# Performance work log

Measured on AMD Instinct MI355X. Metric: run time of the kernel, lower is better.

## Reference

```python
import jax, jax.numpy as jnp
import numpy as np

H, DK, DV, BS = 8, 64, 64, 128


def setup_inputs() -> dict:
    key = jax.random.key(0)
    ks = jax.random.split(key, 6)
    B, T, D = 2, 8193, 1024
    inner = H * DK
    x = jax.random.normal(ks[0], (B, T, D), jnp.float32)
    s = 0.02
    Wq = jax.random.normal(ks[1], (D, inner), jnp.float32) * s
    Wk = jax.random.normal(ks[2], (D, inner), jnp.float32) * s
    Wv = jax.random.normal(ks[3], (D, H * DV), jnp.float32) * s
    Wo = jax.random.normal(ks[4], (H * DV, D), jnp.float32) * s
    bo = jnp.zeros((D,), jnp.float32)
    return {"x": x, "Wq": Wq, "Wk": Wk, "Wv": Wv, "Wo": Wo, "bo": bo}


def _bigbird(x, Wq, Wk, Wv, Wo, bo):
    B, T, D = x.shape
    N = T - 1
    nb = N // BS
    scale = 1.0 / jnp.sqrt(jnp.asarray(DK, x.dtype))
    # projections -> (B, H, T, d)
    q = (x @ Wq).reshape(B, T, H, DK).transpose(0, 2, 1, 3)
    k = (x @ Wk).reshape(B, T, H, DK).transpose(0, 2, 1, 3)
    v = (x @ Wv).reshape(B, T, H, DV).transpose(0, 2, 1, 3)

    # global token (position 0) attends to everything
    sg = jnp.einsum('bhd,bhtd->bht', q[:, :, 0], k) * scale
    pg = jax.nn.softmax(sg, axis=-1)
    out_g = jnp.einsum('bht,bhtd->bhd', pg, v)  # (B,H,DV)

    kg = k[:, :, 0]  # (B,H,DK)
    vg = v[:, :, 0]  # (B,H,DV)
    qx = q[:, :, 1:].reshape(B, H, nb, BS, DK)
    kx = k[:, :, 1:].reshape(B, H, nb, BS, DK)
    vx = v[:, :, 1:].reshape(B, H, nb, BS, DV)

    # zero-pad one block on each side (faithful to original: zero blocks, not masked)
    kp = jnp.pad(kx, ((0, 0), (0, 0), (1, 1), (0, 0), (0, 0)))
    vp = jnp.pad(vx, ((0, 0), (0, 0), (1, 1), (0, 0), (0, 0)))
    k_local = jnp.concatenate([kp[:, :, 0:nb], kp[:, :, 1:nb + 1], kp[:, :, 2:nb + 2]], axis=3)
    v_local = jnp.concatenate([vp[:, :, 0:nb], vp[:, :, 1:nb + 1], vp[:, :, 2:nb + 2]], axis=3)

    kg_e = jnp.broadcast_to(kg[:, :, None, None, :], (B, H, nb, 1, DK))
    vg_e = jnp.broadcast_to(vg[:, :, None, None, :], (B, H, nb, 1, DV))
    k_full = jnp.concatenate([kg_e, k_local], axis=3)  # (B,H,nb,1+3BS,DK)
    v_full = jnp.concatenate([vg_e, v_local], axis=3)

    scores = jnp.einsum('bhnqd,bhnkd->bhnqk', qx, k_full) * scale
    p = jax.nn.softmax(scores, axis=-1)
    out_x = jnp.einsum('bhnqk,bhnkd->bhnqd', p, v_full).reshape(B, H, N, DV)

    out = jnp.concatenate([out_g[:, :, None, :], out_x], axis=2)  # (B,H,T,DV)
    out = out.transpose(0, 2, 1, 3).reshape(B, T, H * DV)
    return out @ Wo + bo


def reference(x, Wq, Wk, Wv, Wo, bo):
    return _bigbird(x, Wq, Wk, Wv, Wo, bo)
```

## Files before the change

### kernel.cpp

```cpp
#include <hip/hip_runtime.h>
#include <hip/hip_bf16.h>

#define T_TOK 8193
#define MROWS 16386
#define NBLK  64
#define GCH   16
#define GCS   513

typedef __attribute__((ext_vector_type(8))) short bf16x8;
typedef __attribute__((ext_vector_type(4))) float f32x4;
typedef unsigned short u16;
typedef unsigned int   u32;

__device__ __forceinline__ float blo(u32 u){ return __uint_as_float(u << 16); }
__device__ __forceinline__ float bhi(u32 u){ return __uint_as_float(u & 0xffff0000u); }
__device__ __forceinline__ u16 f2b(float f){
  u32 u = __float_as_uint(f);
  u = (u + 0x7fffu + ((u >> 16) & 1u)) >> 16;
  return (u16)u;
}
__device__ __forceinline__ float b2f(u16 v){ return __uint_as_float(((u32)v) << 16); }

#define GLDS16(gsrc, ldst) \
  __builtin_amdgcn_global_load_lds((const __attribute__((address_space(1))) void*)(gsrc), \
                                   (__attribute__((address_space(3))) void*)(ldst), 16, 0, 0)

__global__ __launch_bounds__(256)
void convx(const float* __restrict__ x, u16* __restrict__ xb)
{
  const size_t i = (size_t)blockIdx.x * 256 + threadIdx.x;
  const float4* p = (const float4*)x + i * 2;
  float4 a = p[0], b = p[1];
  uint4 st;
  st.x = (u32)f2b(a.x) | ((u32)f2b(a.y) << 16);
  st.y = (u32)f2b(a.z) | ((u32)f2b(a.w) << 16);
  st.z = (u32)f2b(b.x) | ((u32)f2b(b.y) << 16);
  st.w = (u32)f2b(b.z) | ((u32)f2b(b.w) << 16);
  *(uint4*)(xb + i * 8) = st;
}

__global__ __launch_bounds__(256)
void transposeW(const float* __restrict__ B0, const float* __restrict__ B1,
                const float* __restrict__ B2, int bpart,
                u16* __restrict__ outT, int K)
{
  __shared__ float tile[64][65];
  const int n0 = blockIdx.x * 64;
  const int k0 = blockIdx.y * 64;
  const int tx = threadIdx.x & 63;
  const int ty = threadIdx.x >> 6;
  const int part = n0 / bpart;
  const float* Bm = part == 0 ? B0 : (part == 1 ? B1 : B2);
  const int bn = n0 - part * bpart;
  #pragma unroll
  for (int i = 0; i < 16; ++i) {
    int k = i * 4 + ty;
    tile[tx][k] = Bm[(size_t)(k0 + k) * bpart + bn + tx];
  }
  __syncthreads();
  #pragma unroll
  for (int i = 0; i < 16; ++i) {
    int r = i * 4 + ty;
    outT[(size_t)(n0 + r) * K + k0 + tx] = f2b(tile[r][tx]);
  }
}

template<bool OUT_F32>
__global__ __launch_bounds__(512, 4)
void gemmk(const u16* __restrict__ A, const u16* __restrict__ BT,
           void* __restrict__ Cp, const float* __restrict__ bias,
           int M, int K, int ntm, int ntn, int ldc)
{
  __shared__ u16 lds[36864];
  const int tid  = threadIdx.x;
  const int lane = tid & 63;
  const int wid  = tid >> 6;
  const int l15  = lane & 15;
  const int g    = lane >> 4;
  const int wm   = (wid >> 1) * 64;
  const int wn   = (wid & 1) * 64;

  const int nwg  = gridDim.x;
  const int orig = blockIdx.x;
  const int q8 = nwg >> 3, r8 = nwg & 7;
  const int xcd = orig & 7, loc = orig >> 3;
  const int wg = (xcd < r8 ? xcd * (q8 + 1) : r8 * (q8 + 1) + (xcd - r8) * q8) + loc;
  const int GT  = 4;
  const int gsz = GT * ntn;
  const int tg  = wg / gsz;
  const int rem = wg - tg * gsz;
  const int gt  = (ntm - tg * GT < GT) ? (ntm - tg * GT) : GT;
  const int tn  = rem / gt;
  const int tml = rem - tn * gt;
  const int bm0 = (tg * GT + tml) * 256;
  const int bn0 = tn * 128;

  f32x4 acc[4][4];
  #pragma unroll
  for (int i = 0; i < 4; ++i)
    #pragma unroll
    for (int j = 0; j < 4; ++j) { f32x4 z = {0.f,0.f,0.f,0.f}; acc[i][j] = z; }

  const int rr   = tid >> 2;
  const int ch   = tid & 3;
  const int srcq = (ch ^ ((rr >> 1) & 3)) * 8;
  int ar0 = bm0 + rr;        if (ar0 >= M) ar0 = M - 1;
  int ar1 = bm0 + 128 + rr;  if (ar1 >= M) ar1 = M - 1;
  const u32 aOff0 = (u32)ar0 * (u32)K + srcq;
  const u32 aOff1 = (u32)ar1 * (u32)K + srcq;
  const u32 bOff  = (u32)(bn0 + rr) * (u32)K + srcq;
  const int ld8   = tid * 8;

#define STG(BUF, KO) do { \
    GLDS16(A + aOff0 + (KO), &lds[(BUF) * 12288 + ld8]); \
    GLDS16(A + aOff1 + (KO), &lds[(BUF) * 12288 + 4096 + ld8]); \
    GLDS16(BT + bOff + (KO), &lds[(BUF) * 12288 + 8192 + ld8]); \
  } while (0)

  const int ca = (g ^ ((l15 >> 1) & 3)) * 8;

  STG(0, 0);
  STG(1, 32);
  asm volatile("s_waitcnt vmcnt(3)" ::: "memory");
  __builtin_amdgcn_s_barrier();

  const int nt = K >> 5;
  int bufc = 0, bufn = 2;
  for (int t = 0; t < nt; ++t) {
    const int base = bufc * 12288;
    const bool more = (t + 2 < nt);
    bf16x8 bfr[4], af[2];
    #pragma unroll
    for (int ni = 0; ni < 4; ++ni)
      bfr[ni] = *(const bf16x8*)&lds[base + 8192 + (wn + ni * 16 + l15) * 32 + ca];
    af[0] = *(const bf16x8*)&lds[base + (wm + l15) * 32 + ca];
    af[1] = *(const bf16x8*)&lds[base + (wm + 16 + l15) * 32 + ca];
    if (more) STG(bufn, (t + 2) * 32);
    __builtin_amdgcn_s_barrier();
    __builtin_amdgcn_s_setprio(1);
    #pragma unroll
    for (int mi = 0; mi < 2; ++mi)
      #pragma unroll
      for (int ni = 0; ni < 4; ++ni)
        acc[mi][ni] = __builtin_amdgcn_mfma_f32_16x16x32_bf16(af[mi], bfr[ni], acc[mi][ni], 0, 0, 0);
    __builtin_amdgcn_s_setprio(0);
    __builtin_amdgcn_s_barrier();
    af[0] = *(const bf16x8*)&lds[base + (wm + 32 + l15) * 32 + ca];
    af[1] = *(const bf16x8*)&lds[base + (wm + 48 + l15) * 32 + ca];
    __builtin_amdgcn_s_barrier();
    __builtin_amdgcn_s_setprio(1);
    #pragma unroll
    for (int mi = 0; mi < 2; ++mi)
      #pragma unroll
      for (int ni = 0; ni < 4; ++ni)
        acc[2 + mi][ni] = __builtin_amdgcn_mfma_f32_16x16x32_bf16(af[mi], bfr[ni], acc[2 + mi][ni], 0, 0, 0);
    __builtin_amdgcn_s_setprio(0);
    if (more) asm volatile("s_waitcnt vmcnt(3)" ::: "memory");
    else      asm volatile("s_waitcnt vmcnt(0)" ::: "memory");
    __builtin_amdgcn_s_barrier();
    bufc = (bufc + 1 == 3) ? 0 : bufc + 1;
    bufn = (bufn + 1 == 3) ? 0 : bufn + 1;
  }
#undef STG

  #pragma unroll
  for (int mi = 0; mi < 4; ++mi) {
    #pragma unroll
    for (int r = 0; r < 4; ++r) {
      int grow = bm0 + wm + mi * 16 + g * 4 + r;
      if (grow >= M) continue;
      #pragma unroll
      for (int ni = 0; ni < 4; ++ni) {
        int gcol  = bn0 + wn + ni * 16 + l15;
        float val = acc[mi][ni][r];
        if (OUT_F32) ((float*)Cp)[(size_t)grow * ldc + gcol] = val + bias[gcol];
        else         ((u16*)Cp)[(size_t)grow * ldc + gcol]   = f2b(val);
      }
    }
  }
}

__global__ __launch_bounds__(256)
void gsplit(const u16* __restrict__ qkv, float* __restrict__ gbuf)
{
  const int c   = blockIdx.x & 15;
  const int h   = (blockIdx.x >> 4) & 7;
  const int b   = blockIdx.x >> 7;
  const int tid = threadIdx.x;
  const int lane = tid & 63;
  const int wid  = tid >> 6;
  const int t0 = c * GCS;
  const int t1 = (t0 + GCS < T_TOK) ? (t0 + GCS) : T_TOK;
  const int nt = t1 - t0;

  __shared__ float sc[GCS];
  __shared__ float q0s[64];
  __shared__ float wredm[4], wreds[4];
  __shared__ float psum[4][64];

  const size_t base = (size_t)b * T_TOK * 1536;
  if (tid < 32) {
    u32 u = ((const u32*)(qkv + base + h * 64))[tid];
    q0s[2 * tid] = blo(u); q0s[2 * tid + 1] = bhi(u);
  }
  __syncthreads();

  float lmax = -INFINITY;
  for (int tt = tid; tt < nt; tt += 256) {
    const uint4* kp = (const uint4*)(qkv + base + (size_t)(t0 + tt) * 1536 + 512 + h * 64);
    float a = 0.f;
    #pragma unroll
    for (int q8 = 0; q8 < 8; ++q8) {
      uint4 kk = kp[q8];
      a += q0s[q8*8+0]*blo(kk.x) + q0s[q8*8+1]*bhi(kk.x)
         + q0s[q8*8+2]*blo(kk.y) + q0s[q8*8+3]*bhi(kk.y)
         + q0s[q8*8+4]*blo(kk.z) + q0s[q8*8+5]*bhi(kk.z)
         + q0s[q8*8+6]*blo(kk.w) + q0s[q8*8+7]*bhi(kk.w);
    }
    a *= 0.125f;
    sc[tt] = a;
    lmax = fmaxf(lmax, a);
  }
  for (int o = 32; o; o >>= 1) lmax = fmaxf(lmax, __shfl_xor(lmax, o, 64));
  if (lane == 0) wredm[wid] = lmax;
  __syncthreads();
  float bmax = fmaxf(fmaxf(wredm[0], wredm[1]), fmaxf(wredm[2], wredm[3]));
  float lsum = 0.f;
  for (int tt = tid; tt < nt; tt += 256) {
    float e = __expf(sc[tt] - bmax);
    sc[tt] = e;
    lsum += e;
  }
  for (int o = 32; o; o >>= 1) lsum += __shfl_xor(lsum, o, 64);
  if (lane == 0) wreds[wid] = lsum;
  __syncthreads();
  float bsum = wreds[0] + wreds[1] + wreds[2] + wreds[3];

  const int g = tid >> 6;
  const int d = tid & 63;
  float acc = 0.f;
  for (int tt = g; tt < nt; tt += 4)
    acc += sc[tt] * b2f(qkv[base + (size_t)(t0 + tt) * 1536 + 1024 + h * 64 + d]);
  psum[g][d] = acc;
  __syncthreads();

  float* rec = gbuf + ((size_t)(b * 8 + h) * GCH + c) * 66;
  if (tid < 64)
    rec[2 + tid] = psum[0][tid] + psum[1][tid] + psum[2][tid] + psum[3][tid];
  if (tid == 64) { rec[0] = bmax; rec[1] = bsum; }
}

__global__ __launch_bounds__(64)
void gmerge(const float* __restrict__ gbuf, u16* __restrict__ attnb)
{
  const int bh = blockIdx.x;
  const int d  = threadIdx.x;
  const float* recs = gbuf + (size_t)bh * GCH * 66;
  float m = -INFINITY;
  #pragma unroll
  for (int c = 0; c < GCH; ++c) m = fmaxf(m, recs[c * 66]);
  float l = 0.f, o = 0.f;
  #pragma unroll
  for (int c = 0; c < GCH; ++c) {
    float e = __expf(recs[c * 66] - m);
    l += recs[c * 66 + 1] * e;
    o += recs[c * 66 + 2 + d] * e;
  }
  const int b = bh >> 3, h = bh & 7;
  attnb[(size_t)b * T_TOK * 512 + h * 64 + d] = f2b(o / l);
}

__global__ __launch_bounds__(256)
void local_attn_mfma(const u16* __restrict__ qkv, u16* __restrict__ attnb)
{
  const int bid = blockIdx.x;
  const int n = bid & 63;
  const int h = (bid >> 6) & 7;
  const int b = bid >> 9;
  const int tid  = threadIdx.x;
  const int lane = tid & 63;
  const int wid  = tid >> 6;
  const int l15  = lane & 15;
  const int g    = lane >> 4;

  __shared__ u16 K_lds[128 * 72];
  __shared__ u16 V_T[64 * 136];
  __shared__ u16 P_lds[4][32 * 72];
  __shared__ float bb[4][2][32];
  __shared__ float Kg[64], Vg[64];

  const size_t rb = (size_t)b * T_TOK;
  if (tid < 64) {
    Kg[tid] = b2f(qkv[rb * 1536 + 512 + h * 64 + tid]);
    Vg[tid] = b2f(qkv[rb * 1536 + 1024 + h * 64 + tid]);
  }

  const int q0row = 1 + n * 128 + wid * 32;
  bf16x8 qf[2][2];
  #pragma unroll
  for (int qt = 0; qt < 2; ++qt)
    #pragma unroll
    for (int kk = 0; kk < 2; ++kk)
      qf[qt][kk] = *(const bf16x8*)(qkv + (rb + q0row + qt * 16 + l15) * 1536 + h * 64 + kk * 32 + g * 8);

  __syncthreads();

  float sg[2];
  #pragma unroll
  for (int qt = 0; qt < 2; ++qt) {
    float part = 0.f;
    #pragma unroll
    for (int kk = 0; kk < 2; ++kk)
      #pragma unroll
      for (int i = 0; i < 8; ++i)
        part += b2f((u16)qf[qt][kk][i]) * Kg[kk * 32 + g * 8 + i];
    part += __shfl_xor(part, 16, 64);
    part += __shfl_xor(part, 32, 64);
    sg[qt] = part * 0.125f;
  }

  float m[2] = {-INFINITY, -INFINITY};
  float l[2] = {0.f, 0.f};
  f32x4 of[2][4];
  #pragma unroll
  for (int qt = 0; qt < 2; ++qt)
    #pragma unroll
    for (int dt = 0; dt < 4; ++dt) { f32x4 z = {0.f,0.f,0.f,0.f}; of[qt][dt] = z; }

  for (int dblk = 0; dblk < 3; ++dblk) {
    const int blk = n + dblk - 1;
    if (blk < 0 || blk >= NBLK) continue;
    const size_t krow0 = rb + 1 + (size_t)blk * 128;

    __syncthreads();
    #pragma unroll
    for (int it = 0; it < 4; ++it) {
      int c = it * 256 + tid;
      int key = c >> 3, oct = c & 7;
      *(uint4*)&K_lds[key * 72 + oct * 8] =
          *(const uint4*)(qkv + (krow0 + key) * 1536 + 512 + h * 64 + oct * 8);
    }
    #pragma unroll
    for (int it = 0; it < 2; ++it) {
      int c = it * 256 + tid;
      int kp2 = c & 63, oct = c >> 6;
      const u16* s0 = qkv + (krow0 + 2 * kp2) * 1536 + 1024 + h * 64 + oct * 8;
      uint4 va = *(const uint4*)s0;
      uint4 vb4 = *(const uint4*)(s0 + 1536);
      union { uint4 q; u16 hh[8]; } ua, ub;
      ua.q = va; ub.q = vb4;
      #pragma unroll
      for (int i = 0; i < 8; ++i) {
        u32 w = (u32)ua.hh[i] | ((u32)ub.hh[i] << 16);
        *(u32*)&V_T[(oct * 8 + i) * 136 + 2 * kp2] = w;
      }
    }
    __syncthreads();

    f32x4 st[2][8];
    #pragma unroll
    for (int kt = 0; kt < 8; ++kt) {
      bf16x8 kfr[2];
      #pragma unroll
      for (int kk = 0; kk < 2; ++kk)
        kfr[kk] = *(const bf16x8*)&K_lds[(kt * 16 + l15) * 72 + kk * 32 + g * 8];
      #pragma unroll
      for (int qt = 0; qt < 2; ++qt) {
        f32x4 z = {0.f,0.f,0.f,0.f};
        z = __builtin_amdgcn_mfma_f32_16x16x32_bf16(kfr[0], qf[qt][0], z, 0, 0, 0);
        z = __builtin_amdgcn_mfma_f32_16x16x32_bf16(kfr[1], qf[qt][1], z, 0, 0, 0);
        st[qt][kt] = z;
      }
    }
    #pragma unroll
    for (int qt = 0; qt < 2; ++qt) {
      float bm = -INFINITY;
      #pragma unroll
      for (int kt = 0; kt < 8; ++kt)
        #pragma unroll
        for (int r = 0; r < 4; ++r) bm = fmaxf(bm, st[qt][kt][r]);
      bm = fmaxf(bm, __shfl_xor(bm, 16, 64));
      bm = fmaxf(bm, __shfl_xor(bm, 32, 64));
      bm *= 0.125f;
      float mn = fmaxf(m[qt], bm);
      float corr = __expf(m[qt] - mn);
      float bsum = 0.f;
      #pragma unroll
      for (int kt = 0; kt < 8; ++kt)
        #pragma unroll
        for (int r = 0; r < 4; ++r) {
          float p = __expf(__builtin_fmaf(st[qt][kt][r], 0.125f, -mn));
          st[qt][kt][r] = p;
          bsum += p;
        }
      bsum += __shfl_xor(bsum, 16, 64);
      bsum += __shfl_xor(bsum, 32, 64);
      l[qt] = l[qt] * corr + bsum;
      m[qt] = mn;
      if (lane < 16) bb[wid][0][qt * 16 + lane] = corr;
    }
    float rc[2][4];
    #pragma unroll
    for (int qt = 0; qt < 2; ++qt)
      #pragma unroll
      for (int r = 0; r < 4; ++r) rc[qt][r] = bb[wid][0][qt * 16 + g * 4 + r];
    #pragma unroll
    for (int qt = 0; qt < 2; ++qt)
      #pragma unroll
      for (int dt = 0; dt < 4; ++dt)
        #pragma unroll
        for (int r = 0; r < 4; ++r) of[qt][dt][r] *= rc[qt][r];

    u16* P_w = (u16*)P_lds[wid];
    #pragma unroll
    for (int half = 0; half < 2; ++half) {
      #pragma unroll
      for (int qt = 0; qt < 2; ++qt)
        #pragma unroll
        for (int k4 = 0; k4 < 4; ++k4) {
          int kt = half * 4 + k4;
          u16 h0 = f2b(st[qt][kt][0]), h1 = f2b(st[qt][kt][1]);
          u16 h2 = f2b(st[qt][kt][2]), h3 = f2b(st[qt][kt][3]);
          uint2 pk = { (u32)h0 | ((u32)h1 << 16), (u32)h2 | ((u32)h3 << 16) };
          *(uint2*)&P_w[(qt * 16 + l15) * 72 + k4 * 16 + g * 4] = pk;
        }
      #pragma unroll
      for (int ks = 0; ks < 2; ++ks) {
        bf16x8 pa[2];
        #pragma unroll
        for (int qt = 0; qt < 2; ++qt)
          pa[qt] = *(const bf16x8*)&P_w[(qt * 16 + l15) * 72 + ks * 32 + g * 8];
        #pragma unroll
        for (int dt = 0; dt < 4; ++dt) {
          bf16x8 vb = *(const bf16x8*)&V_T[(dt * 16 + l15) * 136 + half * 64 + ks * 32 + g * 8];
          #pragma unroll
          for (int qt = 0; qt < 2; ++qt)
            of[qt][dt] = __builtin_amdgcn_mfma_f32_16x16x32_bf16(pa[qt], vb, of[qt][dt], 0, 0, 0);
        }
      }
    }
  }

  const int nz = (n == 0) + (n == NBLK - 1);
  #pragma unroll
  for (int qt = 0; qt < 2; ++qt) {
    float mf   = fmaxf(m[qt], sg[qt]);
    float corr = __expf(m[qt] - mf);
    float eg   = __expf(sg[qt] - mf);
    float lf   = l[qt] * corr + eg;
    if (nz) lf += (float)(nz * 128) * __expf(-mf);
    float inv = 1.f / lf;
    if (lane < 16) {
      bb[wid][0][qt * 16 + lane] = corr * inv;
      bb[wid][1][qt * 16 + lane] = eg * inv;
    }
  }
  float vgr[4];
  #pragma unroll
  for (int dt = 0; dt < 4; ++dt) vgr[dt] = Vg[dt * 16 + l15];
  #pragma unroll
  for (int qt = 0; qt < 2; ++qt)
    #pragma unroll
    for (int r = 0; r < 4; ++r) {
      float af = bb[wid][0][qt * 16 + g * 4 + r];
      float bf = bb[wid][1][qt * 16 + g * 4 + r];
      int row = q0row + qt * 16 + g * 4 + r;
      u16* dst = attnb + (rb + row) * 512 + h * 64;
      #pragma unroll
      for (int dt = 0; dt < 4; ++dt)
        dst[dt * 16 + l15] = f2b(of[qt][dt][r] * af + bf * vgr[dt]);
    }
}

extern "C" void kernel_launch(void* const* d_in, const int* in_sizes, int n_in,
                              void* d_out, int out_size, void* d_ws, size_t ws_size,
                              hipStream_t stream) {
  (void)in_sizes; (void)n_in; (void)out_size; (void)ws_size;
  const float* x  = (const float*)d_in[0];
  const float* Wq = (const float*)d_in[1];
  const float* Wk = (const float*)d_in[2];
  const float* Wv = (const float*)d_in[3];
  const float* Wo = (const float*)d_in[4];
  const float* bo = (const float*)d_in[5];
  float* out = (float*)d_out;

  char* ws = (char*)d_ws;
  u16* qkv   = (u16*)ws;
  u16* xb    = (u16*)(ws + 50337792);
  u16* attnb = (u16*)(ws + 50337792);
  u16* WoT   = (u16*)(ws + 67117056);
  u16* WqkvT = (u16*)d_out;
  float* gbuf = (float*)((char*)d_out + (4 << 20));

  dim3 blk(256);
  convx<<<dim3(8193), blk, 0, stream>>>(x, xb);
  transposeW<<<dim3(24, 16), blk, 0, stream>>>(Wq, Wk, Wv, 512, WqkvT, 1024);
  gemmk<false><<<dim3(65 * 12), dim3(512), 0, stream>>>(xb, WqkvT, qkv, nullptr, MROWS, 1024, 65, 12, 1536);
  transposeW<<<dim3(16, 8), blk, 0, stream>>>(Wo, Wo, Wo, 1024, WoT, 512);
  gsplit<<<dim3(256), blk, 0, stream>>>(qkv, gbuf);
  gmerge<<<dim3(16), dim3(64), 0, stream>>>(gbuf, attnb);
  local_attn_mfma<<<dim3(1024), blk, 0, stream>>>(qkv, attnb);
  gemmk<true><<<dim3(65 * 8), dim3(512), 0, stream>>>(attnb, WoT, out, bo, MROWS, 512, 65, 8, 1024);
}
```

Baseline: 203.1 us.

## Fuse fp32-to-bf16 conversion of x into the QKV projection GEMM

Removes the separate convx pass that wrote a bf16 copy of x. A new 128x128-tile GEMM loads fp32 x straight into LDS and converts A fragments to bf16 with v_cvt_pk_bf16_f32 before the MFMAs. This saves one full read and write of x (about 67MB fp32), but the GEMM now reads A at twice the byte width, uses smaller tiles with 256 threads, and repeats the conversion for each N tile.

```diff
diff --git a/kernel.cpp b/kernel.cpp
--- a/kernel.cpp
+++ b/kernel.cpp
@@ -20,24 +20,13 @@
   return (u16)u;
 }
 __device__ __forceinline__ float b2f(u16 v){ return __uint_as_float(((u32)v) << 16); }
+__device__ __forceinline__ u32 cvtpk(float lo, float hi){
+  u32 r; asm("v_cvt_pk_bf16_f32 %0, %1, %2" : "=v"(r) : "v"(lo), "v"(hi)); return r;
+}
 
 #define GLDS16(gsrc, ldst) \
   __builtin_amdgcn_global_load_lds((const __attribute__((address_space(1))) void*)(gsrc), \
                                    (__attribute__((address_space(3))) void*)(ldst), 16, 0, 0)
-
-__global__ __launch_bounds__(256)
-void convx(const float* __restrict__ x, u16* __restrict__ xb)
-{
-  const size_t i = (size_t)blockIdx.x * 256 + threadIdx.x;
-  const float4* p = (const float4*)x + i * 2;
-  float4 a = p[0], b = p[1];
-  uint4 st;
-  st.x = (u32)f2b(a.x) | ((u32)f2b(a.y) << 16);
-  st.y = (u32)f2b(a.z) | ((u32)f2b(a.w) << 16);
-  st.z = (u32)f2b(b.x) | ((u32)f2b(b.y) << 16);
-  st.w = (u32)f2b(b.z) | ((u32)f2b(b.w) << 16);
-  *(uint4*)(xb + i * 8) = st;
-}
 
 __global__ __launch_bounds__(256)
 void transposeW(const float* __restrict__ B0, const float* __restrict__ B1,
@@ -62,6 +51,130 @@
   for (int i = 0; i < 16; ++i) {
     int r = i * 4 + ty;
     outT[(size_t)(n0 + r) * K + k0 + tx] = f2b(tile[r][tx]);
+  }
+}
+
+__global__ __launch_bounds__(256, 4)
+void gemmf(const float* __restrict__ X, const u16* __restrict__ BT,
+           u16* __restrict__ C, int M, int K, int ntm, int ntn, int ldc)
+{
+  __shared__ float Af[2][4096];
+  __shared__ u16   Bs[2][4096];
+  const int tid  = threadIdx.x;
+  const int lane = tid & 63;
+  const int wid  = tid >> 6;
+  const int l15  = lane & 15;
+  const int g    = lane >> 4;
+  const int wm   = (wid >> 1) * 64;
+  const int wn   = (wid & 1) * 64;
+
+  const int nwg  = gridDim.x;
+  const int orig = blockIdx.x;
+  const int q8 = nwg >> 3, r8 = nwg & 7;
+  const int xcd = orig & 7, loc = orig >> 3;
+  const int wg = (xcd < r8 ? xcd * (q8 + 1) : r8 * (q8 + 1) + (xcd - r8) * q8) + loc;
+  const int GT  = 8;
+  const int gsz = GT * ntn;
+  const int tg  = wg / gsz;
+  const int rem = wg - tg * gsz;
+  const int gt  = (ntm - tg * GT < GT) ? (ntm - tg * GT) : GT;
+  const int tn  = rem / gt;
+  const int tml = rem - tn * gt;
+  const int bm0 = (tg * GT + tml) * 128;
+  const int bn0 = tn * 128;
+
+  f32x4 acc[4][4];
+  #pragma unroll
+  for (int i = 0; i < 4; ++i)
+    #pragma unroll
+    for (int j = 0; j < 4; ++j) { f32x4 z = {0.f,0.f,0.f,0.f}; acc[i][j] = z; }
+
+  const int srcA = ((tid & 7) ^ ((tid >> 3) & 7)) * 4;
+  u32 aOff[4];
+  #pragma unroll
+  for (int i = 0; i < 4; ++i) {
+    int ar = bm0 + i * 32 + (tid >> 3); if (ar >= M) ar = M - 1;
+    aOff[i] = (u32)ar * (u32)K + srcA;
+  }
+  const int srcB = ((tid & 3) ^ ((tid >> 3) & 3)) * 8;
+  u32 bOff[2];
+  #pragma unroll
+  for (int j = 0; j < 2; ++j)
+    bOff[j] = (u32)(bn0 + j * 64 + (tid >> 2)) * (u32)K + srcB;
+
+#define STG(BUF, T) do { \
+    _Pragma("unroll") for (int i = 0; i < 4; ++i) \
+      GLDS16(X + aOff[i] + (T) * 32, &Af[BUF][(i * 256 + tid) * 4]); \
+    _Pragma("unroll") for (int j = 0; j < 2; ++j) \
+      GLDS16(BT + bOff[j] + (T) * 32, &Bs[BUF][(j * 256 + tid) * 8]); \
+  } while (0)
+
+  const int cab  = (g ^ ((l15 >> 1) & 3)) * 8;
+  const int ca0A = ((2 * g) ^ (l15 & 7)) * 4;
+  const int ca1A = ((2 * g + 1) ^ (l15 & 7)) * 4;
+
+#define AFRAG(DST, BUF, MI) do { \
+    const float* ap = &Af[BUF][(wm + (MI) * 16 + l15) * 32]; \
+    f32x4 x0 = *(const f32x4*)&ap[ca0A]; \
+    f32x4 x1 = *(const f32x4*)&ap[ca1A]; \
+    union { u32 w[4]; bf16x8 v; } uu; \
+    uu.w[0] = cvtpk(x0[0], x0[1]); uu.w[1] = cvtpk(x0[2], x0[3]); \
+    uu.w[2] = cvtpk(x1[0], x1[1]); uu.w[3] = cvtpk(x1[2], x1[3]); \
+    DST = uu.v; \
+  } while (0)
+
+  STG(0, 0);
+  asm volatile("s_waitcnt vmcnt(0)" ::: "memory");
+  __builtin_amdgcn_s_barrier();
+
+  const int nt = K >> 5;
+  for (int t = 0; t < nt; ++t) {
+    const int tb = t & 1;
+    const bool more = (t + 1 < nt);
+    bf16x8 bfr[4], af[2];
+    #pragma unroll
+    for (int ni = 0; ni < 4; ++ni)
+      bfr[ni] = *(const bf16x8*)&Bs[tb][(wn + ni * 16 + l15) * 32 + cab];
+    AFRAG(af[0], tb, 0);
+    AFRAG(af[1], tb, 1);
+    if (more) STG(tb ^ 1, t + 1);
+    __builtin_amdgcn_s_barrier();
+    __builtin_amdgcn_s_setprio(1);
+    #pragma unroll
+    for (int mi = 0; mi < 2; ++mi)
+      #pragma unroll
+      for (int ni = 0; ni < 4; ++ni)
+        acc[mi][ni] = __builtin_amdgcn_mfma_f32_16x16x32_bf16(af[mi], bfr[ni], acc[mi][ni], 0, 0, 0);
+    __builtin_amdgcn_s_setprio(0);
+    __builtin_amdgcn_s_barrier();
+    AFRAG(af[0], tb, 2);
+    AFRAG(af[1], tb, 3);
+    __builtin_amdgcn_s_barrier();
+    __builtin_amdgcn_s_setprio(1);
+    #pragma unroll
+    for (int mi = 0; mi < 2; ++mi)
+      #pragma unroll
+      for (int ni = 0; ni < 4; ++ni)
+        acc[2 + mi][ni] = __builtin_amdgcn_mfma_f32_16x16x32_bf16(af[mi], bfr[ni], acc[2 + mi][ni], 0, 0, 0);
+    __builtin_amdgcn_s_setprio(0);
+    if (more) asm volatile("s_waitcnt vmcnt(0)" ::: "memory");
+    __builtin_amdgcn_s_barrier();
+  }
+#undef STG
+#undef AFRAG
+
+  #pragma unroll
+  for (int mi = 0; mi < 4; ++mi) {
+    #pragma unroll
+    for (int r = 0; r < 4; ++r) {
+      int grow = bm0 + wm + mi * 16 + g * 4 + r;
+      if (grow >= M) continue;
+      #pragma unroll
+      for (int ni = 0; ni < 4; ++ni) {
+        int gcol = bn0 + wn + ni * 16 + l15;
+        C[(size_t)grow * ldc + gcol] = f2b(acc[mi][ni][r]);
+      }
+    }
   }
 }
 
@@ -486,16 +599,14 @@
 
   char* ws = (char*)d_ws;
   u16* qkv   = (u16*)ws;
-  u16* xb    = (u16*)(ws + 50337792);
   u16* attnb = (u16*)(ws + 50337792);
   u16* WoT   = (u16*)(ws + 67117056);
   u16* WqkvT = (u16*)d_out;
   float* gbuf = (float*)((char*)d_out + (4 << 20));
 
   dim3 blk(256);
-  convx<<<dim3(8193), blk, 0, stream>>>(x, xb);
   transposeW<<<dim3(24, 16), blk, 0, stream>>>(Wq, Wk, Wv, 512, WqkvT, 1024);
-  gemmk<false><<<dim3(65 * 12), dim3(512), 0, stream>>>(xb, WqkvT, qkv, nullptr, MROWS, 1024, 65, 12, 1536);
+  gemmf<<<dim3(129 * 12), blk, 0, stream>>>(x, WqkvT, qkv, MROWS, 1024, 129, 12, 1536);
   transposeW<<<dim3(16, 8), blk, 0, stream>>>(Wo, Wo, Wo, 1024, WoT, 512);
   gsplit<<<dim3(256), blk, 0, stream>>>(qkv, gbuf);
   gmerge<<<dim3(16), dim3(64), 0, stream>>>(gbuf, attnb);
```

After: 220.9 us. 8.8% more time.
